# Optimization experiments

Hardware: AMD Instinct MI355X
Metric: run time of the kernel (lower is better)

Reference implementation:

```python
import jax, jax.numpy as jnp
import numpy as np

N_JOINTS = 24

def _rodrigues(r):
    # r: [B, J, 3] axis-angle -> [B, J, 3, 3] rotation matrices
    theta = jnp.clip(jnp.linalg.norm(r, axis=-1, keepdims=True), 1e-6)  # [B,J,1]
    rh = r / theta
    z = jnp.zeros_like(rh[..., :1])
    # skew-symmetric matrix m
    m = jnp.stack([
        jnp.concatenate([z, -rh[..., 2:3], rh[..., 1:2]], -1),
        jnp.concatenate([rh[..., 2:3], z, -rh[..., 0:1]], -1),
        jnp.concatenate([-rh[..., 1:2], rh[..., 0:1], z], -1),
    ], axis=-2)  # [B,J,3,3]
    rrT = rh[..., :, None] * rh[..., None, :]  # outer product [B,J,3,3]
    cos = jnp.cos(theta)[..., None]
    sin = jnp.sin(theta)[..., None]
    eye = jnp.eye(3, dtype=r.dtype)
    return cos * eye + (1.0 - cos) * rrT + sin * m

def _with_zeros(Rm, t):
    # Rm: [B,3,3], t: [B,3] -> [B,4,4] homogeneous transform
    B = Rm.shape[0]
    top = jnp.concatenate([Rm, t[:, :, None]], axis=-1)  # [B,3,4]
    bot = jnp.broadcast_to(jnp.array([0.0, 0.0, 0.0, 1.0], Rm.dtype), (B, 1, 4))
    return jnp.concatenate([top, bot], axis=1)

def _keypoints(v, idx):
    # v: [B,N,3], idx: [G,K] vertex-index groups -> [B,G,3] via (max+min)/2
    g = v[:, idx]  # [B,G,K,3] irregular gather
    return (g.max(axis=2) + g.min(axis=2)) * 0.5

def setup_inputs() -> dict:
    key = jax.random.key(0)
    ks = jax.random.split(key, 8)
    B, N, P, K = 64, 40000, 100, 128
    beta = jax.random.normal(ks[0], (B, P), jnp.float32)
    pose = jax.random.normal(ks[1], (B, N_JOINTS * 3), jnp.float32) * 0.3
    trans = jax.random.normal(ks[2], (B, 3), jnp.float32)
    shapedirs = jax.random.normal(ks[3], (P, 3 * N), jnp.float32) * 0.01
    v_template = jax.random.normal(ks[4], (N, 3), jnp.float32)
    w = jax.random.uniform(ks[5], (N, N_JOINTS), jnp.float32)
    weights = w / w.sum(axis=1, keepdims=True)  # LBS weights sum to 1
    reorder_index = jnp.arange(N_JOINTS, dtype=jnp.int64 if jax.config.jax_enable_x64 else jnp.int32)
    # kinematic tree: parent[i] < i (binary-tree shape stands in for the rabbit skeleton)
    parent = jnp.concatenate([jnp.zeros(1, jnp.int32), (jnp.arange(1, N_JOINTS, dtype=jnp.int32) - 1) // 2])
    joint_idx = jax.random.randint(ks[6], (N_JOINTS - 1, K), 0, N)
    add_idx = jax.random.randint(ks[7], (7, K), 0, N)
    return {"beta": beta, "pose": pose, "trans": trans, "shapedirs": shapedirs,
            "v_template": v_template, "weights": weights, "reorder_index": reorder_index,
            "parent": parent, "joint_idx": joint_idx, "add_idx": add_idx}

def reference(beta, pose, trans, shapedirs, v_template, weights,
              reorder_index, parent, joint_idx, add_idx):
    B = beta.shape[0]
    pose = pose.reshape(B, N_JOINTS, 3)[:, reorder_index]
    # blend shapes: v_shaped = beta @ shapedirs + template
    v_posed = (beta @ shapedirs + v_template.reshape(-1)).reshape(B, -1, 3)  # [B,N,3]
    # joints from vertex-group (max+min)/2, root is zero
    J = jnp.concatenate([jnp.zeros((B, 1, 3), beta.dtype), _keypoints(v_posed, joint_idx)], axis=1)  # [B,24,3]
    R = _rodrigues(pose)  # [B,24,3,3]
    # forward kinematics along the tree (fixed 24-joint loop)
    par = np.asarray(jax.device_get(parent))
    G = [_with_zeros(R[:, 0], J[:, 0])]
    for i in range(1, N_JOINTS):
        p = int(par[i])
        G_loc = _with_zeros(R[:, i], J[:, i] - J[:, p])
        G.append(jnp.matmul(G[p], G_loc))
    G = jnp.stack(G, axis=1)  # [B,24,4,4]
    # remove rest-pose joint locations (pack subtraction only touches last column)
    Jh = jnp.concatenate([J, jnp.zeros((B, N_JOINTS, 1), beta.dtype)], axis=-1)[..., None]  # [B,24,4,1]
    t_corr = jnp.matmul(G, Jh)  # [B,24,4,1]
    G1 = jnp.concatenate([G[..., :3], G[..., 3:4] - t_corr], axis=-1)
    # LBS skinning: per-vertex blended transform
    T = jnp.einsum('nk,bkij->bnij', weights, G1)  # [B,N,4,4]
    vh = jnp.concatenate([v_posed, jnp.ones((B, v_posed.shape[1], 1), beta.dtype)], axis=-1)  # [B,N,4]
    posed = jnp.einsum('bnij,bnj->bni', T, vh)[..., :3] + trans[:, None, :]  # [B,N,3]
    skeleton = jnp.concatenate([
        jnp.zeros((B, 1, 3), beta.dtype),
        _keypoints(posed, joint_idx),
        _keypoints(posed, add_idx),
    ], axis=1)  # [B,31,3]
    return posed, skeleton
```

## Files before the change

### kernel.cpp

```cpp
#include <hip/hip_runtime.h>
#include <math.h>

#define B   64
#define NV  40000
#define P   100
#define KG  128
#define NJ  24
#define TV  16
#define NSK 31
#define NSUB (KG / TV)

typedef __attribute__((ext_vector_type(8))) short bf16x8;
typedef __attribute__((ext_vector_type(4))) float f32x4;

__device__ __forceinline__ unsigned short rne_bf16(float f) {
  unsigned u = __float_as_uint(f);
  u = (u + 0x7FFFu + ((u >> 16) & 1u)) >> 16;
  return (unsigned short)u;
}

__global__ __launch_bounds__(256)
void k_jpart(const float* __restrict__ beta,
             const float* __restrict__ sd,
             const float* __restrict__ vt,
             const int*   __restrict__ joint_idx,
             float*       __restrict__ pmn,
             float*       __restrict__ pmx) {
  const int j = blockIdx.x;
  const int s = blockIdx.y;
  const int t = threadIdx.x;

  __shared__ __align__(16) float beta_s[B * P];
  __shared__ __align__(16) float sd_s[P * TV * 4];
  __shared__ float vt_s[TV][3];
  __shared__ int   idx_s[TV];

  if (t < TV) idx_s[t] = joint_idx[j * KG + s * TV + t];
  for (int e = t; e < B * P; e += 256) beta_s[e] = beta[e];
  __syncthreads();

  for (int e = t; e < P * TV * 3; e += 256) {
    const int p = e / (TV * 3), q = e % (TV * 3);
    const int v = q / 3, c = q % 3;
    sd_s[(p * TV + v) * 4 + c] = sd[(size_t)p * (3 * NV) + (size_t)idx_s[v] * 3 + c];
  }
  if (t < TV * 3) vt_s[t / 3][t % 3] = vt[idx_s[t / 3] * 3 + (t % 3)];
  __syncthreads();

  const int v1 = t & 15;
  const int bg = t >> 4;
  const float4* sd4 = (const float4*)sd_s;
  float acc[4][3];
#pragma unroll
  for (int i = 0; i < 4; ++i)
#pragma unroll
    for (int c = 0; c < 3; ++c) acc[i][c] = 0.0f;
#pragma unroll 2
  for (int p = 0; p < P; ++p) {
    const float4 s4 = sd4[p * TV + v1];
#pragma unroll
    for (int i = 0; i < 4; ++i) {
      const float bb = beta_s[(bg * 4 + i) * P + p];
      acc[i][0] += bb * s4.x;
      acc[i][1] += bb * s4.y;
      acc[i][2] += bb * s4.z;
    }
  }
  float mn[4][3], mx[4][3];
#pragma unroll
  for (int i = 0; i < 4; ++i)
#pragma unroll
    for (int c = 0; c < 3; ++c) {
      const float v = acc[i][c] + vt_s[v1][c];
      mn[i][c] = v; mx[i][c] = v;
    }
#pragma unroll
  for (int off = 1; off < 16; off <<= 1) {
#pragma unroll
    for (int i = 0; i < 4; ++i)
#pragma unroll
      for (int c = 0; c < 3; ++c) {
        mn[i][c] = fminf(mn[i][c], __shfl_xor(mn[i][c], off));
        mx[i][c] = fmaxf(mx[i][c], __shfl_xor(mx[i][c], off));
      }
  }
  if (v1 == 0) {
#pragma unroll
    for (int i = 0; i < 4; ++i) {
      const int b = bg * 4 + i;
#pragma unroll
      for (int c = 0; c < 3; ++c) {
        pmn[((j * NSUB + s) * B + b) * 3 + c] = mn[i][c];
        pmx[((j * NSUB + s) * B + b) * 3 + c] = mx[i][c];
      }
    }
  }
}

__global__ void k_chain(const float* __restrict__ pose,
                        const int*   __restrict__ parent,
                        const float* __restrict__ pmn,
                        const float* __restrict__ pmx,
                        const float* __restrict__ beta,
                        const float* __restrict__ trans,
                        unsigned short* __restrict__ G1A,
                        unsigned short* __restrict__ beta_bf) {
  const int b = blockIdx.x;
  const int t = threadIdx.x;

  __shared__ float R[NJ][9];
  __shared__ float Jl[NJ][3];
  __shared__ float G[NJ][12];
  __shared__ float G1c[NJ][12];

  if (t < NJ) {
    const float x = pose[b * NJ * 3 + t * 3 + 0];
    const float y = pose[b * NJ * 3 + t * 3 + 1];
    const float z = pose[b * NJ * 3 + t * 3 + 2];
    const float th = fmaxf(sqrtf(x * x + y * y + z * z), 1e-6f);
    const float xh = x / th, yh = y / th, zh = z / th;
    const float c = cosf(th), s = sinf(th), o = 1.0f - c;
    R[t][0] = c + o * xh * xh;      R[t][1] = o * xh * yh - s * zh; R[t][2] = o * xh * zh + s * yh;
    R[t][3] = o * xh * yh + s * zh; R[t][4] = c + o * yh * yh;      R[t][5] = o * yh * zh - s * xh;
    R[t][6] = o * xh * zh - s * yh; R[t][7] = o * yh * zh + s * xh; R[t][8] = c + o * zh * zh;
    if (t == 0) {
      Jl[0][0] = 0.0f; Jl[0][1] = 0.0f; Jl[0][2] = 0.0f;
    } else {
      const int jj = t - 1;
#pragma unroll
      for (int c2 = 0; c2 < 3; ++c2) {
        float lo = 1e30f, hi = -1e30f;
#pragma unroll
        for (int s2 = 0; s2 < NSUB; ++s2) {
          lo = fminf(lo, pmn[((jj * NSUB + s2) * B + b) * 3 + c2]);
          hi = fmaxf(hi, pmx[((jj * NSUB + s2) * B + b) * 3 + c2]);
        }
        Jl[t][c2] = 0.5f * (lo + hi);
      }
    }
  }
  __syncthreads();

  if (t < 12) {
    const int r = t >> 2, c = t & 3;
    G[0][t] = (c < 3) ? R[0][r * 3 + c] : Jl[0][r];
  }
  __syncthreads();

  for (int i = 1; i < NJ; ++i) {
    const int p = parent[i];
    if (t < 12) {
      const int r = t >> 2, c = t & 3;
      const float g0 = G[p][r * 4 + 0];
      const float g1 = G[p][r * 4 + 1];
      const float g2 = G[p][r * 4 + 2];
      float l0, l1, l2, add;
      if (c < 3) {
        l0 = R[i][0 * 3 + c]; l1 = R[i][1 * 3 + c]; l2 = R[i][2 * 3 + c];
        add = 0.0f;
      } else {
        l0 = Jl[i][0] - Jl[p][0]; l1 = Jl[i][1] - Jl[p][1]; l2 = Jl[i][2] - Jl[p][2];
        add = G[p][r * 4 + 3];
      }
      G[i][t] = g0 * l0 + g1 * l1 + g2 * l2 + add;
    }
    __syncthreads();
  }

  for (int e = t; e < NJ * 12; e += 64) {
    const int i = e / 12, rc = e % 12, r = rc >> 2, c = rc & 3;
    float val;
    if (c < 3) {
      val = G[i][rc];
    } else {
      val = G[i][r * 4 + 3] - (G[i][r * 4 + 0] * Jl[i][0] +
                               G[i][r * 4 + 1] * Jl[i][1] +
                               G[i][r * 4 + 2] * Jl[i][2]);
    }
    G1c[i][rc] = val;
  }
  __syncthreads();

  for (int e = t; e < 136; e += 64)
    beta_bf[b * 136 + e] = (e < P) ? rne_bf16(beta[b * P + e]) : (unsigned short)0;

  for (int e = t; e < 512; e += 64) {
    const int m = e >> 5, k = e & 31;
    float val = 0.0f;
    if (m < 12) {
      if (k < NJ) val = G1c[k][m];
      else if (k == NJ && (m & 3) == 3) val = trans[b * 3 + (m >> 2)];
    }
    G1A[(size_t)b * 512 + e] = rne_bf16(val);
  }
}

__global__ __launch_bounds__(256)
void k_skin(const float* __restrict__ sd,
            const float* __restrict__ vt,
            const float* __restrict__ w,
            const unsigned short* __restrict__ beta_bf,
            const unsigned short* __restrict__ G1A,
            float*       __restrict__ out) {
  const int n0v = blockIdx.x * TV;
  const int col0 = n0v * 3;
  const int t  = threadIdx.x;
  const int lane = t & 63, wv = t >> 6;
  const int l15 = lane & 15, q = lane >> 4;

  __shared__ __align__(16) unsigned short beta_s[64 * 136];
  __shared__ __align__(16) unsigned short sdT_s[48 * 136];
  __shared__ __align__(16) unsigned short wT_s[16 * 40];
  __shared__ float vt_s[48];
  float* vhf  = (float*)beta_s;
  float* pos_s = (float*)sdT_s;

  for (int e = t; e < 64 * 136 / 8; e += 256)
    ((uint4*)beta_s)[e] = ((const uint4*)beta_bf)[e];
  for (int task = t; task < 768; task += 256) {
    const int n = task % 48, kg = task / 48;
    unsigned pk[4];
#pragma unroll
    for (int h = 0; h < 4; ++h) {
      const int k0 = kg * 8 + 2 * h;
      float f0 = 0.0f, f1 = 0.0f;
      if (k0 < P)     f0 = sd[(size_t)k0 * (3 * NV) + col0 + n];
      if (k0 + 1 < P) f1 = sd[(size_t)(k0 + 1) * (3 * NV) + col0 + n];
      pk[h] = (unsigned)rne_bf16(f0) | ((unsigned)rne_bf16(f1) << 16);
    }
    *(uint4*)&sdT_s[n * 136 + kg * 8] = make_uint4(pk[0], pk[1], pk[2], pk[3]);
  }
  for (int e = t; e < 512; e += 256) {
    const int n = e >> 5, k = e & 31;
    float val = (k < NJ) ? w[(n0v + n) * NJ + k] : (k == NJ ? 1.0f : 0.0f);
    wT_s[n * 40 + k] = rne_bf16(val);
  }
  if (t < 48) vt_s[t] = vt[col0 + t];
  __syncthreads();

  bf16x8 af[4];
#pragma unroll
  for (int ks = 0; ks < 4; ++ks)
    af[ks] = *(const bf16x8*)&beta_s[(wv * 16 + l15) * 136 + ks * 32 + q * 8];
  f32x4 acc[3];
#pragma unroll
  for (int nt = 0; nt < 3; ++nt) acc[nt] = (f32x4){0.f, 0.f, 0.f, 0.f};
#pragma unroll
  for (int ks = 0; ks < 4; ++ks) {
#pragma unroll
    for (int nt = 0; nt < 3; ++nt) {
      const bf16x8 bf = *(const bf16x8*)&sdT_s[(nt * 16 + l15) * 136 + ks * 32 + q * 8];
      acc[nt] = __builtin_amdgcn_mfma_f32_16x16x32_bf16(af[ks], bf, acc[nt], 0, 0, 0);
    }
  }
  float vtv[3];
#pragma unroll
  for (int nt = 0; nt < 3; ++nt) vtv[nt] = vt_s[nt * 16 + l15];
  __syncthreads();

#pragma unroll
  for (int nt = 0; nt < 3; ++nt) {
    const int n = nt * 16 + l15;
    const int v = n / 3, c = n - 3 * v;
#pragma unroll
    for (int r = 0; r < 4; ++r) {
      const int m = wv * 16 + q * 4 + r;
      vhf[m * 68 + v * 4 + c] = acc[nt][r] + vtv[nt];
    }
  }
  __syncthreads();

  const bf16x8 wf = *(const bf16x8*)&wT_s[l15 * 40 + q * 8];
  const f32x4 zero = (f32x4){0.f, 0.f, 0.f, 0.f};
#pragma unroll 4
  for (int bi = 0; bi < 16; ++bi) {
    const int b = wv * 16 + bi;
    const bf16x8 gf = *(const bf16x8*)&G1A[(size_t)b * 512 + l15 * 32 + q * 8];
    const f32x4 d = __builtin_amdgcn_mfma_f32_16x16x32_bf16(gf, wf, zero, 0, 0, 0);
    const float4 vh = *(const float4*)&vhf[b * 68 + l15 * 4];
    if (q < 3) {
      const float pos = d[0] * vh.x + d[1] * vh.y + d[2] * vh.z + d[3];
      pos_s[b * 48 + l15 * 3 + q] = pos;
    }
  }
  __syncthreads();

  for (int e = t; e < 768; e += 256) {
    const int b = e / 12, ch = e % 12;
    const float4 val = *(const float4*)&pos_s[b * 48 + ch * 4];
    *(float4*)&out[(size_t)b * (NV * 3) + col0 + ch * 4] = val;
  }
}

__global__ void k_skel(const float* __restrict__ posed,
                       const int*   __restrict__ joint_idx,
                       const int*   __restrict__ add_idx,
                       float*       __restrict__ skel) {
  const int j = blockIdx.x;
  const int b = blockIdx.y;
  const int t = threadIdx.x;
  const int idx = (j < 23) ? joint_idx[j * KG + t] : add_idx[(j - 23) * KG + t];

  const float* p = posed + (size_t)b * NV * 3 + (size_t)idx * 3;
  float mn[3], mx[3];
#pragma unroll
  for (int c = 0; c < 3; ++c) { mn[c] = p[c]; mx[c] = p[c]; }
#pragma unroll
  for (int off = 32; off > 0; off >>= 1) {
#pragma unroll
    for (int c = 0; c < 3; ++c) {
      mn[c] = fminf(mn[c], __shfl_down(mn[c], off));
      mx[c] = fmaxf(mx[c], __shfl_down(mx[c], off));
    }
  }
  __shared__ float s_mn[2][3], s_mx[2][3];
  const int wave = t >> 6, lane = t & 63;
  if (lane == 0) {
#pragma unroll
    for (int c = 0; c < 3; ++c) { s_mn[wave][c] = mn[c]; s_mx[wave][c] = mx[c]; }
  }
  __syncthreads();
  if (t == 0) {
#pragma unroll
    for (int c = 0; c < 3; ++c) {
      float lo = fminf(s_mn[0][c], s_mn[1][c]);
      float hi = fmaxf(s_mx[0][c], s_mx[1][c]);
      skel[(b * NSK + 1 + j) * 3 + c] = 0.5f * (lo + hi);
      if (j == 0) skel[(b * NSK + 0) * 3 + c] = 0.0f;
    }
  }
}

extern "C" void kernel_launch(void* const* d_in, const int* in_sizes, int n_in,
                              void* d_out, int out_size, void* d_ws, size_t ws_size,
                              hipStream_t stream) {
  const float* beta     = (const float*)d_in[0];
  const float* pose     = (const float*)d_in[1];
  const float* trans    = (const float*)d_in[2];
  const float* sd       = (const float*)d_in[3];
  const float* vt       = (const float*)d_in[4];
  const float* w        = (const float*)d_in[5];
  const int* parent     = (const int*)d_in[7];
  const int* joint_idx  = (const int*)d_in[8];
  const int* add_idx    = (const int*)d_in[9];

  float* out = (float*)d_out;
  unsigned short* G1A     = (unsigned short*)d_ws;
  unsigned short* beta_bf = G1A + B * 512;
  float* pmn = (float*)(beta_bf + B * 136);
  float* pmx = pmn + 23 * NSUB * B * 3;

  k_jpart<<<dim3(23, NSUB), 256, 0, stream>>>(beta, sd, vt, joint_idx, pmn, pmx);
  k_chain<<<B, 64, 0, stream>>>(pose, parent, pmn, pmx, beta, trans, G1A, beta_bf);
  k_skin <<<NV / TV, 256, 0, stream>>>(sd, vt, w, beta_bf, G1A, out);
  k_skel <<<dim3(30, B), 128, 0, stream>>>(out, joint_idx, add_idx,
                                           out + (size_t)B * NV * 3);
}
```

Baseline: 166.2 us.

## Compute joint-keypoint shape blend with bf16 MFMA instead of FP32 FMA loop

```diff
diff --git a/kernel.cpp b/kernel.cpp
--- a/kernel.cpp
+++ b/kernel.cpp
@@ -29,71 +29,85 @@
   const int j = blockIdx.x;
   const int s = blockIdx.y;
   const int t = threadIdx.x;
-
-  __shared__ __align__(16) float beta_s[B * P];
-  __shared__ __align__(16) float sd_s[P * TV * 4];
-  __shared__ float vt_s[TV][3];
+  const int lane = t & 63, wv = t >> 6;
+  const int l15 = lane & 15, qd = lane >> 4;
+
+  __shared__ __align__(16) unsigned short beta_s[64 * 136];
+  __shared__ __align__(16) unsigned short sdT_s[48 * 136];
+  __shared__ float vt_s[48];
   __shared__ int   idx_s[TV];
+  float* pos_s = (float*)beta_s;
 
   if (t < TV) idx_s[t] = joint_idx[j * KG + s * TV + t];
-  for (int e = t; e < B * P; e += 256) beta_s[e] = beta[e];
-  __syncthreads();
-
-  for (int e = t; e < P * TV * 3; e += 256) {
-    const int p = e / (TV * 3), q = e % (TV * 3);
-    const int v = q / 3, c = q % 3;
-    sd_s[(p * TV + v) * 4 + c] = sd[(size_t)p * (3 * NV) + (size_t)idx_s[v] * 3 + c];
-  }
-  if (t < TV * 3) vt_s[t / 3][t % 3] = vt[idx_s[t / 3] * 3 + (t % 3)];
-  __syncthreads();
-
-  const int v1 = t & 15;
-  const int bg = t >> 4;
-  const float4* sd4 = (const float4*)sd_s;
-  float acc[4][3];
-#pragma unroll
-  for (int i = 0; i < 4; ++i)
-#pragma unroll
-    for (int c = 0; c < 3; ++c) acc[i][c] = 0.0f;
-#pragma unroll 2
-  for (int p = 0; p < P; ++p) {
-    const float4 s4 = sd4[p * TV + v1];
-#pragma unroll
-    for (int i = 0; i < 4; ++i) {
-      const float bb = beta_s[(bg * 4 + i) * P + p];
-      acc[i][0] += bb * s4.x;
-      acc[i][1] += bb * s4.y;
-      acc[i][2] += bb * s4.z;
-    }
-  }
-  float mn[4][3], mx[4][3];
-#pragma unroll
-  for (int i = 0; i < 4; ++i)
-#pragma unroll
-    for (int c = 0; c < 3; ++c) {
-      const float v = acc[i][c] + vt_s[v1][c];
-      mn[i][c] = v; mx[i][c] = v;
-    }
-#pragma unroll
-  for (int off = 1; off < 16; off <<= 1) {
-#pragma unroll
-    for (int i = 0; i < 4; ++i)
-#pragma unroll
-      for (int c = 0; c < 3; ++c) {
-        mn[i][c] = fminf(mn[i][c], __shfl_xor(mn[i][c], off));
-        mx[i][c] = fmaxf(mx[i][c], __shfl_xor(mx[i][c], off));
-      }
-  }
-  if (v1 == 0) {
-#pragma unroll
-    for (int i = 0; i < 4; ++i) {
-      const int b = bg * 4 + i;
-#pragma unroll
-      for (int c = 0; c < 3; ++c) {
-        pmn[((j * NSUB + s) * B + b) * 3 + c] = mn[i][c];
-        pmx[((j * NSUB + s) * B + b) * 3 + c] = mx[i][c];
-      }
-    }
+  __syncthreads();
+
+  for (int e = t; e < 64 * 36; e += 256) {
+    const int m = e / 36, pp = P + e % 36;
+    beta_s[m * 136 + pp] = 0;
+  }
+  for (int e = t; e < 64 * P; e += 256) {
+    const int m = e / P, p = e % P;
+    beta_s[m * 136 + p] = rne_bf16(beta[e]);
+  }
+  for (int task = t; task < 768; task += 256) {
+    const int n = task % 48, kg = task / 48;
+    const size_t colbase = (size_t)idx_s[n / 3] * 3 + (n % 3);
+    unsigned pk[4];
+#pragma unroll
+    for (int h = 0; h < 4; ++h) {
+      const int k0 = kg * 8 + 2 * h;
+      float f0 = 0.0f, f1 = 0.0f;
+      if (k0 < P)     f0 = sd[(size_t)k0 * (3 * NV) + colbase];
+      if (k0 + 1 < P) f1 = sd[(size_t)(k0 + 1) * (3 * NV) + colbase];
+      pk[h] = (unsigned)rne_bf16(f0) | ((unsigned)rne_bf16(f1) << 16);
+    }
+    *(uint4*)&sdT_s[n * 136 + kg * 8] = make_uint4(pk[0], pk[1], pk[2], pk[3]);
+  }
+  if (t < 48) vt_s[t] = vt[(size_t)idx_s[t / 3] * 3 + (t % 3)];
+  __syncthreads();
+
+  bf16x8 af[4];
+#pragma unroll
+  for (int ks = 0; ks < 4; ++ks)
+    af[ks] = *(const bf16x8*)&beta_s[(wv * 16 + l15) * 136 + ks * 32 + qd * 8];
+  f32x4 acc[3];
+#pragma unroll
+  for (int nt = 0; nt < 3; ++nt) acc[nt] = (f32x4){0.f, 0.f, 0.f, 0.f};
+#pragma unroll
+  for (int ks = 0; ks < 4; ++ks) {
+#pragma unroll
+    for (int nt = 0; nt < 3; ++nt) {
+      const bf16x8 bf = *(const bf16x8*)&sdT_s[(nt * 16 + l15) * 136 + ks * 32 + qd * 8];
+      acc[nt] = __builtin_amdgcn_mfma_f32_16x16x32_bf16(af[ks], bf, acc[nt], 0, 0, 0);
+    }
+  }
+  float vtv[3];
+#pragma unroll
+  for (int nt = 0; nt < 3; ++nt) vtv[nt] = vt_s[nt * 16 + l15];
+  __syncthreads();
+
+#pragma unroll
+  for (int nt = 0; nt < 3; ++nt) {
+    const int n = nt * 16 + l15;
+    const int v = n / 3, c = n - 3 * v;
+#pragma unroll
+    for (int r = 0; r < 4; ++r) {
+      const int m = wv * 16 + qd * 4 + r;
+      pos_s[m * 68 + v * 4 + c] = acc[nt][r] + vtv[nt];
+    }
+  }
+  __syncthreads();
+
+  if (t < 192) {
+    const int b = t / 3, c = t % 3;
+    float lo = 1e30f, hi = -1e30f;
+#pragma unroll
+    for (int v = 0; v < TV; ++v) {
+      const float val = pos_s[b * 68 + v * 4 + c];
+      lo = fminf(lo, val); hi = fmaxf(hi, val);
+    }
+    pmn[((j * NSUB + s) * B + b) * 3 + c] = lo;
+    pmx[((j * NSUB + s) * B + b) * 3 + c] = hi;
   }
 }
 
```

New measurement: 156.6 us. 1.06x faster.
